# Kernel tuning notes

Hardware: AMD Instinct MI355X
Metric: run time of the kernel (lower is better)

Reference implementation:

```python
import jax, jax.numpy as jnp
import numpy as np

HIDDEN = 4096
N_HEADS = 32
HEAD_DIM = HIDDEN // N_HEADS  # 128
ROTARY_DIM = 64
ROPE_THETA = 10000.0
B, S = 2, 2048


def setup_inputs() -> dict:
    key = jax.random.key(0)
    k1, k2, k3 = jax.random.split(key, 3)
    hidden_states = jax.random.normal(k1, (B, S, HIDDEN), dtype=jnp.float32)
    positions = jnp.broadcast_to(jnp.arange(S, dtype=jnp.int32), (B, S))
    Wqkv = jax.random.normal(k2, (HIDDEN, 3 * HIDDEN), dtype=jnp.float32) * 0.02
    Wout = jax.random.normal(k3, (HIDDEN, HIDDEN), dtype=jnp.float32) * 0.02
    return {"hidden_states": hidden_states, "positions": positions,
            "Wqkv": Wqkv, "Wout": Wout}


def _apply_rope_neox(x, positions):
    # x: [B, S, H, D]; rotate first ROTARY_DIM dims, neox style (half split)
    half = ROTARY_DIM // 2
    inv_freq = 1.0 / (ROPE_THETA ** (jnp.arange(0, half, dtype=jnp.float32) * 2.0 / ROTARY_DIM))
    angles = positions.astype(jnp.float32)[..., None] * inv_freq  # [B, S, half]
    cos = jnp.cos(angles)[:, :, None, :]  # [B, S, 1, half]
    sin = jnp.sin(angles)[:, :, None, :]
    x_rot, x_pass = x[..., :ROTARY_DIM], x[..., ROTARY_DIM:]
    x1, x2 = x_rot[..., :half], x_rot[..., half:]
    o1 = x1 * cos - x2 * sin
    o2 = x2 * cos + x1 * sin
    return jnp.concatenate([o1, o2, x_pass], axis=-1)


def reference(hidden_states, positions, Wqkv, Wout):
    # fused QKV projection (no bias)
    qkv = jnp.einsum('bsh,hk->bsk', hidden_states, Wqkv)  # [B, S, 3H]
    q, k, v = jnp.split(qkv, 3, axis=-1)
    q = q.reshape(B, S, N_HEADS, HEAD_DIM)
    k = k.reshape(B, S, N_HEADS, HEAD_DIM)
    v = v.reshape(B, S, N_HEADS, HEAD_DIM)
    q = _apply_rope_neox(q, positions)
    k = _apply_rope_neox(k, positions)
    scale = HEAD_DIM ** -0.5
    scores = jnp.einsum('bqhd,bkhd->bhqk', q, k) * scale  # [B, H, S, S]
    causal = jnp.tril(jnp.ones((S, S), dtype=bool))
    scores = jnp.where(causal, scores, jnp.finfo(scores.dtype).min)
    probs = jax.nn.softmax(scores, axis=-1)
    attn = jnp.einsum('bhqk,bkhd->bqhd', probs, v).reshape(B, S, HIDDEN)
    return jnp.einsum('bsh,ho->bso', attn, Wout)
```

## Files before the change

### kernel.cpp

```cpp
#include <hip/hip_runtime.h>
#include <hip/hip_bf16.h>

#define HIDDEN 4096
#define NHEADS 32
#define HEADDIM 128
#define ROT 64
#define BB 2
#define SS 2048
#define NTOK (BB*SS)
#define QKVN (3*HIDDEN)

typedef __attribute__((ext_vector_type(8))) short short8;
typedef __attribute__((ext_vector_type(4))) float floatx4;

__global__ void cast_bf16_kernel(const float* __restrict__ x,
                                 __hip_bfloat16* __restrict__ y, int n4) {
  int idx = blockIdx.x * blockDim.x + threadIdx.x;
  if (idx >= n4) return;
  float4 v = ((const float4*)x)[idx];
  __hip_bfloat162 a, b;
  a.x = __float2bfloat16(v.x); a.y = __float2bfloat16(v.y);
  b.x = __float2bfloat16(v.z); b.y = __float2bfloat16(v.w);
  ((__hip_bfloat162*)y)[idx * 2]     = a;
  ((__hip_bfloat162*)y)[idx * 2 + 1] = b;
}

__device__ inline void store_val(float* p, float v) { *p = v; }
__device__ inline void store_val(__hip_bfloat16* p, float v) { *p = __float2bfloat16(v); }

template <typename OutT>
__global__ __launch_bounds__(256) void gemm_kernel(const __hip_bfloat16* __restrict__ A,
                                                   const float* __restrict__ B,
                                                   OutT* __restrict__ C,
                                                   int M, int N, int K) {
  __shared__ __hip_bfloat16 As[128 * 40];
  __shared__ __hip_bfloat16 Bs[128 * 40];
  const int tid  = threadIdx.x;
  const int wid  = tid >> 6;
  const int lane = tid & 63;
  const int quad = lane >> 4;
  const int l16  = lane & 15;
  const int wm   = (wid >> 1) * 64;
  const int wn   = (wid & 1) * 64;
  const int m0   = blockIdx.y * 128;
  const int n0   = blockIdx.x * 128;

  floatx4 acc[4][4] = {};

  for (int kb = 0; kb < K; kb += 32) {
    __syncthreads();
#pragma unroll
    for (int i = 0; i < 2; ++i) {
      int c   = tid + i * 256;
      int row = c >> 2;
      int kc  = (c & 3) * 8;
      short8 av = *(const short8*)(A + (size_t)(m0 + row) * K + kb + kc);
      *(short8*)(As + row * 40 + kc) = av;
    }
#pragma unroll
    for (int i = 0; i < 8; ++i) {
      int c = tid + i * 256;
      int n = c & 127;
      int k = (c >> 7) * 2;
      const float* g = B + (size_t)(kb + k) * N + n0 + n;
      __hip_bfloat162 p;
      p.x = __float2bfloat16(g[0]);
      p.y = __float2bfloat16(g[N]);
      *(__hip_bfloat162*)(Bs + n * 40 + k) = p;
    }
    __syncthreads();

    short8 af[4], bf[4];
#pragma unroll
    for (int t = 0; t < 4; ++t)
      af[t] = *(const short8*)(As + (wm + t * 16 + l16) * 40 + quad * 8);
#pragma unroll
    for (int t = 0; t < 4; ++t)
      bf[t] = *(const short8*)(Bs + (wn + t * 16 + l16) * 40 + quad * 8);
#pragma unroll
    for (int mi = 0; mi < 4; ++mi)
#pragma unroll
      for (int ni = 0; ni < 4; ++ni)
        acc[mi][ni] = __builtin_amdgcn_mfma_f32_16x16x32_bf16(af[mi], bf[ni], acc[mi][ni], 0, 0, 0);
  }

#pragma unroll
  for (int mi = 0; mi < 4; ++mi)
#pragma unroll
    for (int ni = 0; ni < 4; ++ni)
#pragma unroll
      for (int r = 0; r < 4; ++r) {
        int row = m0 + wm + mi * 16 + quad * 4 + r;
        int col = n0 + wn + ni * 16 + l16;
        store_val(C + (size_t)row * N + col, acc[mi][ni][r]);
      }
}

__global__ void rope_kernel(__hip_bfloat16* __restrict__ qkv,
                            const int* __restrict__ positions) {
  int idx = blockIdx.x * blockDim.x + threadIdx.x;
  if (idx >= NTOK * NHEADS * (ROT / 2)) return;
  int i   = idx & 31;
  int h   = (idx >> 5) & 31;
  int tok = idx >> 10;
  float pos = (float)positions[tok];
  float inv_freq = __expf(-(float)i * 0.28782313662425574f);
  float ang = pos * inv_freq;
  float sv, cv;
  sincosf(ang, &sv, &cv);
  size_t base = (size_t)tok * QKVN + h * HEADDIM + i;
  {
    float x1 = __bfloat162float(qkv[base]);
    float x2 = __bfloat162float(qkv[base + 32]);
    qkv[base]      = __float2bfloat16(x1 * cv - x2 * sv);
    qkv[base + 32] = __float2bfloat16(x2 * cv + x1 * sv);
  }
  {
    float x1 = __bfloat162float(qkv[base + HIDDEN]);
    float x2 = __bfloat162float(qkv[base + HIDDEN + 32]);
    qkv[base + HIDDEN]      = __float2bfloat16(x1 * cv - x2 * sv);
    qkv[base + HIDDEN + 32] = __float2bfloat16(x2 * cv + x1 * sv);
  }
}

__global__ __launch_bounds__(256) void attn_kernel(const __hip_bfloat16* __restrict__ qkv,
                                                   __hip_bfloat16* __restrict__ out) {
  __shared__ __hip_bfloat16 QPs[64 * 136];
  __shared__ __hip_bfloat16 Ks[64 * 136];
  __shared__ __hip_bfloat16 Vt[128 * 72];

  const int tid  = threadIdx.x;
  const int wid  = tid >> 6;
  const int lane = tid & 63;
  const int quad = lane >> 4;
  const int l16  = lane & 15;
  const int qt   = 31 - (blockIdx.x & 31);
  const int h    = (blockIdx.x >> 5) & 31;
  const int b    = blockIdx.x >> 10;
  const int qtok0 = b * SS + qt * 64;
  const float scale = 0.08838834764831843f;

#pragma unroll
  for (int i = 0; i < 4; ++i) {
    int c = tid + i * 256;
    int row = c >> 4;
    int dc  = (c & 15) * 8;
    short8 v = *(const short8*)(qkv + (size_t)(qtok0 + row) * QKVN + h * HEADDIM + dc);
    *(short8*)(QPs + row * 136 + dc) = v;
  }
  __syncthreads();
  short8 aq[4];
#pragma unroll
  for (int kc = 0; kc < 4; ++kc)
    aq[kc] = *(const short8*)(QPs + (wid * 16 + l16) * 136 + kc * 32 + quad * 8);

  float m_r[4], l_r[4];
  floatx4 accO[8];
#pragma unroll
  for (int r = 0; r < 4; ++r) { m_r[r] = -INFINITY; l_r[r] = 0.f; }
#pragma unroll
  for (int ni = 0; ni < 8; ++ni) accO[ni] = (floatx4){0.f, 0.f, 0.f, 0.f};

  __hip_bfloat16* Ps = QPs;

  for (int kt = 0; kt <= qt; ++kt) {
    __syncthreads();
    const int ktok = b * SS + kt * 64;

#pragma unroll
    for (int i = 0; i < 4; ++i) {
      int c = tid + i * 256;
      int row = c >> 4;
      int dc  = (c & 15) * 8;
      short8 v = *(const short8*)(qkv + (size_t)(ktok + row) * QKVN + HIDDEN + h * HEADDIM + dc);
      *(short8*)(Ks + row * 136 + dc) = v;
    }
#pragma unroll
    for (int i = 0; i < 8; ++i) {
      int c  = tid + i * 256;
      int dp = (c & 7) | ((c >> 3) & 0x38);
      int kp = ((c >> 3) & 7) | ((c >> 6) & 0x18);
      const __hip_bfloat16* g = qkv + (size_t)(ktok + 2 * kp) * QKVN + 2 * HIDDEN + h * HEADDIM + 2 * dp;
      __hip_bfloat162 v0 = *(const __hip_bfloat162*)g;
      __hip_bfloat162 v1 = *(const __hip_bfloat162*)(g + QKVN);
      __hip_bfloat162 w0, w1;
      w0.x = v0.x; w0.y = v1.x;
      w1.x = v0.y; w1.y = v1.y;
      *(__hip_bfloat162*)(Vt + (2 * dp) * 72 + 2 * kp)     = w0;
      *(__hip_bfloat162*)(Vt + (2 * dp + 1) * 72 + 2 * kp) = w1;
    }
    __syncthreads();

    floatx4 accS[4] = {};
#pragma unroll
    for (int ni = 0; ni < 4; ++ni)
#pragma unroll
      for (int kc = 0; kc < 4; ++kc) {
        short8 bk = *(const short8*)(Ks + (16 * ni + l16) * 136 + kc * 32 + quad * 8);
        accS[ni] = __builtin_amdgcn_mfma_f32_16x16x32_bf16(aq[kc], bk, accS[ni], 0, 0, 0);
      }

    float sv[4][4];
#pragma unroll
    for (int ni = 0; ni < 4; ++ni)
#pragma unroll
      for (int r = 0; r < 4; ++r) sv[ni][r] = accS[ni][r] * scale;
    if (kt == qt) {
#pragma unroll
      for (int ni = 0; ni < 4; ++ni)
#pragma unroll
        for (int r = 0; r < 4; ++r)
          if (16 * ni + l16 > wid * 16 + quad * 4 + r) sv[ni][r] = -INFINITY;
    }
#pragma unroll
    for (int r = 0; r < 4; ++r) {
      float mx = fmaxf(fmaxf(sv[0][r], sv[1][r]), fmaxf(sv[2][r], sv[3][r]));
      mx = fmaxf(mx, __shfl_xor(mx, 1));
      mx = fmaxf(mx, __shfl_xor(mx, 2));
      mx = fmaxf(mx, __shfl_xor(mx, 4));
      mx = fmaxf(mx, __shfl_xor(mx, 8));
      float mnew  = fmaxf(m_r[r], mx);
      float alpha = __expf(m_r[r] - mnew);
      float psum = 0.f;
#pragma unroll
      for (int ni = 0; ni < 4; ++ni) {
        float p = __expf(sv[ni][r] - mnew);
        psum += p;
        Ps[(wid * 16 + quad * 4 + r) * 72 + 16 * ni + l16] = __float2bfloat16(p);
      }
      psum += __shfl_xor(psum, 1);
      psum += __shfl_xor(psum, 2);
      psum += __shfl_xor(psum, 4);
      psum += __shfl_xor(psum, 8);
      l_r[r] = l_r[r] * alpha + psum;
      m_r[r] = mnew;
#pragma unroll
      for (int ni = 0; ni < 8; ++ni) accO[ni][r] *= alpha;
    }

    short8 ap[2];
#pragma unroll
    for (int kc = 0; kc < 2; ++kc)
      ap[kc] = *(const short8*)(Ps + (wid * 16 + l16) * 72 + kc * 32 + quad * 8);
#pragma unroll
    for (int ni = 0; ni < 8; ++ni)
#pragma unroll
      for (int kc = 0; kc < 2; ++kc) {
        short8 bv = *(const short8*)(Vt + (16 * ni + l16) * 72 + kc * 32 + quad * 8);
        accO[ni] = __builtin_amdgcn_mfma_f32_16x16x32_bf16(ap[kc], bv, accO[ni], 0, 0, 0);
      }
  }

  float inv_l[4];
#pragma unroll
  for (int r = 0; r < 4; ++r) inv_l[r] = 1.0f / l_r[r];
#pragma unroll
  for (int ni = 0; ni < 8; ++ni)
#pragma unroll
    for (int r = 0; r < 4; ++r) {
      int row = qtok0 + wid * 16 + quad * 4 + r;
      int col = h * HEADDIM + 16 * ni + l16;
      out[(size_t)row * HIDDEN + col] = __float2bfloat16(accO[ni][r] * inv_l[r]);
    }
}

extern "C" void kernel_launch(void* const* d_in, const int* in_sizes, int n_in,
                              void* d_out, int out_size, void* d_ws, size_t ws_size,
                              hipStream_t stream) {
  const float* hidden    = (const float*)d_in[0];
  const int*   positions = (const int*)d_in[1];
  const float* Wqkv      = (const float*)d_in[2];
  const float* Wout      = (const float*)d_in[3];
  float* out = (float*)d_out;

  const size_t XB_BYTES   = (size_t)NTOK * HIDDEN * 2;
  const size_t QKV_BYTES  = (size_t)NTOK * QKVN * 2;
  const size_t AB_BYTES   = (size_t)NTOK * HIDDEN * 2;
  if (ws_size < XB_BYTES + QKV_BYTES + AB_BYTES) return;

  char* ws = (char*)d_ws;
  __hip_bfloat16* Xb   = (__hip_bfloat16*)ws;
  __hip_bfloat16* QKVb = (__hip_bfloat16*)(ws + XB_BYTES);
  __hip_bfloat16* Ab   = (__hip_bfloat16*)(ws + XB_BYTES + QKV_BYTES);

  cast_bf16_kernel<<<(NTOK * HIDDEN / 4 + 255) / 256, 256, 0, stream>>>(
      hidden, Xb, NTOK * HIDDEN / 4);
  gemm_kernel<__hip_bfloat16><<<dim3(QKVN / 128, NTOK / 128), 256, 0, stream>>>(
      Xb, Wqkv, QKVb, NTOK, QKVN, HIDDEN);
  rope_kernel<<<(NTOK * NHEADS * (ROT / 2) + 255) / 256, 256, 0, stream>>>(QKVb, positions);
  attn_kernel<<<BB * NHEADS * (SS / 64), 256, 0, stream>>>(QKVb, Ab);
  gemm_kernel<float><<<dim3(HIDDEN / 128, NTOK / 128), 256, 0, stream>>>(
      Ab, Wout, out, NTOK, HIDDEN, HIDDEN);
}
```

Measured before the change: 1.646 ms.

## Pre-transpose weights to bf16 and stage GEMM tiles with async global-to-LDS loads

Adds a pass that casts the fp32 weights to bf16 and transposes them (K-contiguous) in workspace before each projection GEMM. The GEMM then loads both A and B tiles with 16-byte global_load_lds direct-to-LDS copies instead of strided scalar fp32 loads with conversion in the inner loop. The aim is to cut redundant weight reads and conversions, since each B element was reloaded and converted by every M-block. The trade-offs are extra transpose kernels and workspace, unpadded LDS rows that may cause bank conflicts, and a chunked fallback path when workspace is small.

Measured after the change: 1.459 ms. -11.4%, faster.

```diff
diff --git a/kernel.cpp b/kernel.cpp
--- a/kernel.cpp
+++ b/kernel.cpp
@@ -1,5 +1,6 @@
 #include <hip/hip_runtime.h>
 #include <hip/hip_bf16.h>
+#include <stdint.h>
 
 #define HIDDEN 4096
 #define NHEADS 32
@@ -12,6 +13,13 @@
 
 typedef __attribute__((ext_vector_type(8))) short short8;
 typedef __attribute__((ext_vector_type(4))) float floatx4;
+
+__device__ __forceinline__ void async16(const __hip_bfloat16* g, unsigned lds_byte_addr) {
+  __builtin_amdgcn_global_load_lds(
+      (const __attribute__((address_space(1))) unsigned int*)(uintptr_t)g,
+      (__attribute__((address_space(3))) unsigned int*)(uintptr_t)(uint64_t)lds_byte_addr,
+      16, 0, 0);
+}
 
 __global__ void cast_bf16_kernel(const float* __restrict__ x,
                                  __hip_bfloat16* __restrict__ y, int n4) {
@@ -25,16 +33,36 @@
   ((__hip_bfloat162*)y)[idx * 2 + 1] = b;
 }
 
+__global__ void transpose_cast_kernel(const float* __restrict__ W,
+                                      __hip_bfloat16* __restrict__ Wt,
+                                      int K, int ldn, int n_off) {
+  int n  = blockIdx.x * 256 + threadIdx.x;
+  int k0 = blockIdx.y * 32;
+  const float* src = W + (size_t)k0 * ldn + n_off + n;
+  short8 outv[4];
+#pragma unroll
+  for (int i = 0; i < 4; ++i) {
+#pragma unroll
+    for (int j = 0; j < 8; ++j) {
+      __hip_bfloat16 b = __float2bfloat16(src[(size_t)(i * 8 + j) * ldn]);
+      outv[i][j] = *reinterpret_cast<short*>(&b);
+    }
+  }
+  __hip_bfloat16* dst = Wt + (size_t)n * K + k0;
+#pragma unroll
+  for (int i = 0; i < 4; ++i) *(short8*)(dst + i * 8) = outv[i];
+}
+
 __device__ inline void store_val(float* p, float v) { *p = v; }
 __device__ inline void store_val(__hip_bfloat16* p, float v) { *p = __float2bfloat16(v); }
 
 template <typename OutT>
-__global__ __launch_bounds__(256) void gemm_kernel(const __hip_bfloat16* __restrict__ A,
-                                                   const float* __restrict__ B,
-                                                   OutT* __restrict__ C,
-                                                   int M, int N, int K) {
-  __shared__ __hip_bfloat16 As[128 * 40];
-  __shared__ __hip_bfloat16 Bs[128 * 40];
+__global__ __launch_bounds__(256) void gemm_bt_kernel(const __hip_bfloat16* __restrict__ A,
+                                                      const __hip_bfloat16* __restrict__ Bt,
+                                                      OutT* __restrict__ C,
+                                                      int M, int K, int ldc) {
+  __shared__ __hip_bfloat16 As[128 * 32];
+  __shared__ __hip_bfloat16 Bs[128 * 32];
   const int tid  = threadIdx.x;
   const int wid  = tid >> 6;
   const int lane = tid & 63;
@@ -45,38 +73,33 @@
   const int m0   = blockIdx.y * 128;
   const int n0   = blockIdx.x * 128;
 
+  const int srow = lane >> 2;
+  const int scol = (lane & 3) * 8;
+
+  const unsigned as0 = (unsigned)(uintptr_t)(&As[0]);
+  const unsigned bs0 = (unsigned)(uintptr_t)(&Bs[0]);
+
   floatx4 acc[4][4] = {};
 
   for (int kb = 0; kb < K; kb += 32) {
     __syncthreads();
 #pragma unroll
-    for (int i = 0; i < 2; ++i) {
-      int c   = tid + i * 256;
-      int row = c >> 2;
-      int kc  = (c & 3) * 8;
-      short8 av = *(const short8*)(A + (size_t)(m0 + row) * K + kb + kc);
-      *(short8*)(As + row * 40 + kc) = av;
-    }
-#pragma unroll
-    for (int i = 0; i < 8; ++i) {
-      int c = tid + i * 256;
-      int n = c & 127;
-      int k = (c >> 7) * 2;
-      const float* g = B + (size_t)(kb + k) * N + n0 + n;
-      __hip_bfloat162 p;
-      p.x = __float2bfloat16(g[0]);
-      p.y = __float2bfloat16(g[N]);
-      *(__hip_bfloat162*)(Bs + n * 40 + k) = p;
+    for (int j = 0; j < 2; ++j) {
+      int rblk = wid * 32 + j * 16;
+      unsigned la = __builtin_amdgcn_readfirstlane(as0 + rblk * 64);
+      async16(A + (size_t)(m0 + rblk + srow) * K + kb + scol, la);
+      unsigned lb = __builtin_amdgcn_readfirstlane(bs0 + rblk * 64);
+      async16(Bt + (size_t)(n0 + rblk + srow) * K + kb + scol, lb);
     }
     __syncthreads();
 
     short8 af[4], bf[4];
 #pragma unroll
     for (int t = 0; t < 4; ++t)
-      af[t] = *(const short8*)(As + (wm + t * 16 + l16) * 40 + quad * 8);
+      af[t] = *(const short8*)(As + (wm + t * 16 + l16) * 32 + quad * 8);
 #pragma unroll
     for (int t = 0; t < 4; ++t)
-      bf[t] = *(const short8*)(Bs + (wn + t * 16 + l16) * 40 + quad * 8);
+      bf[t] = *(const short8*)(Bs + (wn + t * 16 + l16) * 32 + quad * 8);
 #pragma unroll
     for (int mi = 0; mi < 4; ++mi)
 #pragma unroll
@@ -92,7 +115,7 @@
       for (int r = 0; r < 4; ++r) {
         int row = m0 + wm + mi * 16 + quad * 4 + r;
         int col = n0 + wn + ni * 16 + l16;
-        store_val(C + (size_t)row * N + col, acc[mi][ni][r]);
+        store_val(C + (size_t)row * ldc + col, acc[mi][ni][r]);
       }
 }
 
@@ -273,22 +296,45 @@
   const float* Wout      = (const float*)d_in[3];
   float* out = (float*)d_out;
 
-  const size_t XB_BYTES   = (size_t)NTOK * HIDDEN * 2;
-  const size_t QKV_BYTES  = (size_t)NTOK * QKVN * 2;
-  const size_t AB_BYTES   = (size_t)NTOK * HIDDEN * 2;
-  if (ws_size < XB_BYTES + QKV_BYTES + AB_BYTES) return;
+  const size_t R0_BYTES      = (size_t)NTOK * HIDDEN * 2;
+  const size_t QKV_BYTES     = (size_t)NTOK * QKVN * 2;
+  const size_t WT_FULL_BYTES = (size_t)QKVN * HIDDEN * 2;
+  const size_t WT_CHUNK_BYTES= (size_t)HIDDEN * HIDDEN * 2;
+
+  const size_t WS_FULL  = R0_BYTES + WT_FULL_BYTES + QKV_BYTES;
+  const size_t WS_CHUNK = R0_BYTES + WT_CHUNK_BYTES + QKV_BYTES;
+  if (ws_size < WS_CHUNK) return;
+  const bool full = (ws_size >= WS_FULL);
 
   char* ws = (char*)d_ws;
   __hip_bfloat16* Xb   = (__hip_bfloat16*)ws;
-  __hip_bfloat16* QKVb = (__hip_bfloat16*)(ws + XB_BYTES);
-  __hip_bfloat16* Ab   = (__hip_bfloat16*)(ws + XB_BYTES + QKV_BYTES);
+  __hip_bfloat16* Ab   = (__hip_bfloat16*)ws;
+  __hip_bfloat16* Wt   = (__hip_bfloat16*)(ws + R0_BYTES);
+  __hip_bfloat16* QKVb = (__hip_bfloat16*)(ws + R0_BYTES + (full ? WT_FULL_BYTES : WT_CHUNK_BYTES));
 
   cast_bf16_kernel<<<(NTOK * HIDDEN / 4 + 255) / 256, 256, 0, stream>>>(
       hidden, Xb, NTOK * HIDDEN / 4);
-  gemm_kernel<__hip_bfloat16><<<dim3(QKVN / 128, NTOK / 128), 256, 0, stream>>>(
-      Xb, Wqkv, QKVb, NTOK, QKVN, HIDDEN);
+
+  if (full) {
+    transpose_cast_kernel<<<dim3(QKVN / 256, HIDDEN / 32), 256, 0, stream>>>(
+        Wqkv, Wt, HIDDEN, QKVN, 0);
+    gemm_bt_kernel<__hip_bfloat16><<<dim3(QKVN / 128, NTOK / 128), 256, 0, stream>>>(
+        Xb, Wt, QKVb, NTOK, HIDDEN, QKVN);
+  } else {
+    for (int p = 0; p < 3; ++p) {
+      transpose_cast_kernel<<<dim3(HIDDEN / 256, HIDDEN / 32), 256, 0, stream>>>(
+          Wqkv, Wt, HIDDEN, QKVN, p * HIDDEN);
+      gemm_bt_kernel<__hip_bfloat16><<<dim3(HIDDEN / 128, NTOK / 128), 256, 0, stream>>>(
+          Xb, Wt, QKVb + p * HIDDEN, NTOK, HIDDEN, QKVN);
+    }
+  }
+
   rope_kernel<<<(NTOK * NHEADS * (ROT / 2) + 255) / 256, 256, 0, stream>>>(QKVb, positions);
+
   attn_kernel<<<BB * NHEADS * (SS / 64), 256, 0, stream>>>(QKVb, Ab);
-  gemm_kernel<float><<<dim3(HIDDEN / 128, NTOK / 128), 256, 0, stream>>>(
-      Ab, Wout, out, NTOK, HIDDEN, HIDDEN);
-}
+
+  transpose_cast_kernel<<<dim3(HIDDEN / 256, HIDDEN / 32), 256, 0, stream>>>(
+      Wout, Wt, HIDDEN, HIDDEN, 0);
+  gemm_bt_kernel<float><<<dim3(HIDDEN / 128, NTOK / 128), 256, 0, stream>>>(
+      Ab, Wt, out, NTOK, HIDDEN, HIDDEN);
+}
```
